# Performance work log

Hardware: AMD Instinct MI355X
Metric: run time of the kernel (lower is better)

The kernel has to match this reference:

```python
import jax, jax.numpy as jnp
import numpy as np

N = 8192
D_IN = 2048
D_OUT = 2048


def _xavier(key, fan_in, fan_out):
    limit = float(np.sqrt(6.0 / (fan_in + fan_out)))
    return jax.random.uniform(key, (fan_in, fan_out), jnp.float32, -limit, limit)


def setup_inputs() -> dict:
    key = jax.random.key(0)
    kx, kk, kv, kq = jax.random.split(key, 4)
    x = jax.random.normal(kx, (N, D_IN), dtype=jnp.float32)
    w_keys = _xavier(kk, D_IN, D_OUT)
    w_values = _xavier(kv, D_IN, D_OUT)
    w_querys = _xavier(kq, D_IN, D_OUT)
    return {"x": x, "w_keys": w_keys, "w_values": w_values, "w_querys": w_querys}


def reference(x, w_keys, w_values, w_querys):
    # QKV projections: [N, d_out]
    keys = x @ w_keys
    values = x @ w_values
    querys = x @ w_querys
    # attn_scores[i, j] = <query_i, key_j>; softmax over keys (last dim)
    attn = jax.nn.softmax(querys @ keys.T, axis=-1)  # [N, N]
    # Original: (values[:,None] * attn.T[:,:,None]).sum(0) == attn @ values
    outputs = attn @ values  # [N, d_out]
    return outputs
```

## Files before the change

### kernel.cpp

```cpp
#include <hip/hip_runtime.h>
#include <hip/hip_bf16.h>
#include <cstdint>
#include <cstddef>


typedef float  f32x4 __attribute__((ext_vector_type(4)));
typedef short  s16x8 __attribute__((ext_vector_type(8)));
typedef unsigned short u16;
typedef u16    u16x4 __attribute__((ext_vector_type(4)));

#define NROWS 8192
#define DDIM  2048

static __device__ __forceinline__ u16 f2bf(float f) {
    unsigned u = __float_as_uint(f);
    u += 0x7FFFu + ((u >> 16) & 1u);
    return (u16)(u >> 16);
}
static __device__ __forceinline__ float bf2f(u16 h) {
    return __uint_as_float(((unsigned)h) << 16);
}
static __device__ __forceinline__ f32x4 mfma16(s16x8 a, s16x8 b, f32x4 c) {
    return __builtin_amdgcn_mfma_f32_16x16x32_bf16(a, b, c, 0, 0, 0);
}

__global__ __launch_bounds__(256) void transpose_f32k(const float* __restrict__ in,
                                                      float* __restrict__ op,
                                                      int rows, int cols) {
    __shared__ float t[32][33];
    const int r  = threadIdx.x >> 3;
    const int c4 = (threadIdx.x & 7) << 2;
    f32x4 v = *(const f32x4*)(in + (size_t)(blockIdx.y * 32 + r) * cols + blockIdx.x * 32 + c4);
    t[r][c4 + 0] = v[0]; t[r][c4 + 1] = v[1]; t[r][c4 + 2] = v[2]; t[r][c4 + 3] = v[3];
    __syncthreads();
    f32x4 o;
#pragma unroll
    for (int j = 0; j < 4; ++j) o[j] = t[c4 + j][r];
    *(f32x4*)(op + (size_t)(blockIdx.x * 32 + r) * rows + blockIdx.y * 32 + c4) = o;
}

__global__ void fill_marker(float* o, long n) {
    long i = (long)blockIdx.x * blockDim.x + threadIdx.x;
    const long stride = (long)gridDim.x * blockDim.x;
    for (; i < n; i += stride) o[i] = 1.0e30f;
}

template<int NA, int NB, int ORD, int AF32, int BF32, int OUTM>
__global__ __launch_bounds__(256) void gemm_u(
    const void* Ap0, const void* Ap1, const void* Ap2, long lda,
    const void* Bp0, const void* Bp1, const void* Bp2, long ldb,
    float* __restrict__ Cf, u16* __restrict__ Ct, long ldc, int K)
{
    __shared__ __align__(16) u16 lds[NA + NB][128][40];

    const int tid  = threadIdx.x;
    const int lane = tid & 63;
    const int w    = tid >> 6;
    const int wr   = w >> 1, wc = w & 1;
    const int lrow = lane & 15, kg = lane >> 4;
    const long brow = (long)blockIdx.y * 128;
    const long bcol = (long)blockIdx.x * 128;
    const int srow = tid >> 1;
    const int sk   = (tid & 1) * 16;

    f32x4 acc[4][4];
#pragma unroll
    for (int m = 0; m < 4; ++m)
#pragma unroll
        for (int n = 0; n < 4; ++n) acc[m][n] = (f32x4){0.f, 0.f, 0.f, 0.f};

    const int nk = K / 32;
    for (int kt = 0; kt < nk; ++kt) {
        u16x4 sa[NA][4], sb[NB][4];
        if (AF32) {
            const float* pA = (const float*)Ap0 + (brow + srow) * lda + (long)kt * 32 + sk;
#pragma unroll
            for (int q = 0; q < 4; ++q) {
                f32x4 v = *(const f32x4*)(pA + q * 4);
#pragma unroll
                for (int e = 0; e < 4; ++e) {
                    float f = v[e];
                    u16 hh = f2bf(f); sa[0][q][e] = hh;
                    if (NA > 1) {
                        float r1 = f - bf2f(hh);
                        u16 mm = f2bf(r1); sa[1][q][e] = mm;
                        if (NA > 2) sa[2][q][e] = f2bf(r1 - bf2f(mm));
                    }
                }
            }
        } else {
            const u16* as[3] = {(const u16*)Ap0, (const u16*)Ap1, (const u16*)Ap2};
            const long off = (brow + srow) * lda + (long)kt * 32 + sk;
#pragma unroll
            for (int i = 0; i < NA; ++i) {
                s16x8 v0 = *(const s16x8*)(as[i] + off);
                s16x8 v1 = *(const s16x8*)(as[i] + off + 8);
                *(s16x8*)&sa[i][0] = v0;
                *(s16x8*)&sa[i][2] = v1;
            }
        }
        if (BF32) {
            const float* pB = (const float*)Bp0 + (bcol + srow) * ldb + (long)kt * 32 + sk;
#pragma unroll
            for (int q = 0; q < 4; ++q) {
                f32x4 v = *(const f32x4*)(pB + q * 4);
#pragma unroll
                for (int e = 0; e < 4; ++e) {
                    float f = v[e];
                    u16 hh = f2bf(f); sb[0][q][e] = hh;
                    if (NB > 1) {
                        float r1 = f - bf2f(hh);
                        u16 mm = f2bf(r1); sb[1][q][e] = mm;
                        if (NB > 2) sb[2][q][e] = f2bf(r1 - bf2f(mm));
                    }
                }
            }
        } else {
            const u16* bs[3] = {(const u16*)Bp0, (const u16*)Bp1, (const u16*)Bp2};
            const long off = (bcol + srow) * ldb + (long)kt * 32 + sk;
#pragma unroll
            for (int j = 0; j < NB; ++j) {
                s16x8 v0 = *(const s16x8*)(bs[j] + off);
                s16x8 v1 = *(const s16x8*)(bs[j] + off + 8);
                *(s16x8*)&sb[j][0] = v0;
                *(s16x8*)&sb[j][2] = v1;
            }
        }

        __syncthreads();
#pragma unroll
        for (int i = 0; i < NA; ++i)
#pragma unroll
            for (int q = 0; q < 4; ++q)
                *(u16x4*)&lds[i][srow][sk + q * 4] = sa[i][q];
#pragma unroll
        for (int j = 0; j < NB; ++j)
#pragma unroll
            for (int q = 0; q < 4; ++q)
                *(u16x4*)&lds[NA + j][srow][sk + q * 4] = sb[j][q];
        __syncthreads();

        s16x8 bfr[NB][4];
#pragma unroll
        for (int j = 0; j < NB; ++j)
#pragma unroll
            for (int n = 0; n < 4; ++n)
                bfr[j][n] = *(const s16x8*)&lds[NA + j][wc * 64 + n * 16 + lrow][kg * 8];
#pragma unroll
        for (int m = 0; m < 4; ++m) {
            s16x8 afr[NA];
#pragma unroll
            for (int i = 0; i < NA; ++i)
                afr[i] = *(const s16x8*)&lds[i][wr * 64 + m * 16 + lrow][kg * 8];
#pragma unroll
            for (int n = 0; n < 4; ++n) {
#pragma unroll
                for (int i = 0; i < NA; ++i)
#pragma unroll
                    for (int j = 0; j < NB; ++j)
                        if (i + j <= ORD)
                            acc[m][n] = mfma16(afr[i], bfr[j][n], acc[m][n]);
            }
        }
    }

#pragma unroll
    for (int m = 0; m < 4; ++m) {
#pragma unroll
        for (int n = 0; n < 4; ++n) {
            const long c = bcol + wc * 64 + n * 16 + lrow;
            if (OUTM == 0) {
#pragma unroll
                for (int reg = 0; reg < 4; ++reg) {
                    const long r = brow + wr * 64 + m * 16 + kg * 4 + reg;
                    Cf[r * ldc + c] = acc[m][n][reg];
                }
            } else {
                const long r0 = brow + wr * 64 + m * 16 + kg * 4;
                u16x4 hv;
#pragma unroll
                for (int reg = 0; reg < 4; ++reg) hv[reg] = f2bf(acc[m][n][reg]);
                *(u16x4*)(Ct + c * ldc + r0) = hv;
            }
        }
    }
}

__global__ __launch_bounds__(256) void softmax_rows(float* __restrict__ S) {
    __shared__ float row[NROWS];
    __shared__ float red[4];
    const int tid = threadIdx.x;
    const int lane = tid & 63, wid = tid >> 6;
    float* src = S + (size_t)blockIdx.x * NROWS;

    float lmax = -3.4e38f;
    for (int i = tid * 4; i < NROWS; i += 1024) {
        f32x4 v = *(const f32x4*)(src + i);
        row[i] = v[0]; row[i + 1] = v[1]; row[i + 2] = v[2]; row[i + 3] = v[3];
        lmax = fmaxf(fmaxf(fmaxf(lmax, v[0]), v[1]), fmaxf(v[2], v[3]));
    }
#pragma unroll
    for (int off = 32; off; off >>= 1) lmax = fmaxf(lmax, __shfl_xor(lmax, off, 64));
    if (lane == 0) red[wid] = lmax;
    __syncthreads();
    const float m = fmaxf(fmaxf(red[0], red[1]), fmaxf(red[2], red[3]));
    __syncthreads();

    float lsum = 0.f;
    for (int i = tid * 4; i < NROWS; i += 1024) {
        float e0 = __expf(row[i] - m);
        float e1 = __expf(row[i + 1] - m);
        float e2 = __expf(row[i + 2] - m);
        float e3 = __expf(row[i + 3] - m);
        row[i] = e0; row[i + 1] = e1; row[i + 2] = e2; row[i + 3] = e3;
        lsum += (e0 + e1) + (e2 + e3);
    }
#pragma unroll
    for (int off = 32; off; off >>= 1) lsum += __shfl_xor(lsum, off, 64);
    if (lane == 0) red[wid] = lsum;
    __syncthreads();
    const float inv = 1.0f / ((red[0] + red[1]) + (red[2] + red[3]));

    u16* ph = (u16*)src;
    for (int i = tid * 4; i < NROWS; i += 1024) {
        u16x4 h;
#pragma unroll
        for (int j = 0; j < 4; ++j) h[j] = f2bf(row[i + j] * inv);
        *(u16x4*)(ph + i) = h;
    }
}

extern "C" void kernel_launch(void* const* d_in, const int* in_sizes, int n_in,
                              void* d_out, int out_size, void* d_ws, size_t ws_size,
                              hipStream_t stream) {
    const float* x  = (const float*)d_in[0];
    const float* wk = (const float*)d_in[1];
    const float* wv = (const float*)d_in[2];
    const float* wq = (const float*)d_in[3];
    float* out = (float*)d_out;
    char*  ws  = (char*)d_ws;
    const size_t MiB = 1024ull * 1024ull;

    long R = 0;
    const size_t fixed = 48 * MiB;
    if      (ws_size >= fixed + 256 * MiB) R = 8192;
    else if (ws_size >= fixed + 128 * MiB) R = 4096;
    else if (ws_size >= fixed +  64 * MiB) R = 2048;
    else if (ws_size >= fixed +  32 * MiB) R = 1024;
    else if (ws_size >= fixed +  16 * MiB) R = 512;
    else if (ws_size >= fixed +   8 * MiB) R = 256;
    if (R == 0) {
        fill_marker<<<dim3(2048), dim3(256), 0, stream>>>(out, (long)NROWS * DDIM);
        return;
    }

    float* Mb  = (float*)(ws);
    u16*   Vt  = (u16*)(ws + 16 * MiB);
    char*  cb  = ws + 48 * MiB;
    float* WvT = (float*)cb;
    float* Sch = (float*)cb;
    float* y   = out;

    const dim3 b256(256);

    gemm_u<3, 3, 2, 1, 1, 0><<<dim3(16, 16), b256, 0, stream>>>(
        wk, nullptr, nullptr, (long)DDIM, wq, nullptr, nullptr, (long)DDIM,
        Mb, nullptr, (long)DDIM, DDIM);

    transpose_f32k<<<dim3(64, 64), b256, 0, stream>>>(wv, WvT, DDIM, DDIM);
    gemm_u<2, 2, 1, 1, 1, 1><<<dim3(16, 64), b256, 0, stream>>>(
        x, nullptr, nullptr, (long)DDIM, WvT, nullptr, nullptr, (long)DDIM,
        nullptr, Vt, (long)NROWS, DDIM);

    gemm_u<2, 2, 1, 1, 1, 0><<<dim3(16, 64), b256, 0, stream>>>(
        x, nullptr, nullptr, (long)DDIM, Mb, nullptr, nullptr, (long)DDIM,
        y, nullptr, (long)DDIM, DDIM);

    const long nc = NROWS / R;
    for (long c = 0; c < nc; ++c) {
        float* yc = y   + (size_t)c * R * DDIM;
        float* oc = out + (size_t)c * R * DDIM;
        gemm_u<2, 2, 1, 1, 1, 0><<<dim3(64, R / 128), b256, 0, stream>>>(
            yc, nullptr, nullptr, (long)DDIM, x, nullptr, nullptr, (long)DDIM,
            Sch, nullptr, (long)NROWS, DDIM);
        softmax_rows<<<dim3(R), b256, 0, stream>>>(Sch);
        gemm_u<1, 1, 0, 0, 0, 0><<<dim3(16, R / 128), b256, 0, stream>>>(
            (const u16*)Sch, nullptr, nullptr, (long)(2 * NROWS),
            Vt, nullptr, nullptr, (long)NROWS,
            oc, nullptr, (long)DDIM, NROWS);
    }
}
```

Baseline: 2.336 ms.

## Pre-split fp32 operands into packed bf16 hi/lo tiles loaded via global_load_lds

Adds pre-pass kernels that split x and the transposed Wv into bf16 high/low pairs stored in an MFMA-fragment-friendly tiled layout. A new GEMM streams these tiles straight into LDS with global_load_lds, which removes the per-iteration fp32-to-bf16 splitting and the register staging. The Wk·Wq product drops from a 3-term to a 2-term split and is written directly in the packed format, and y is stored packed inside the output buffer. This removes repeated conversion work on x across several GEMMs, at the cost of slightly lower precision in the Wk·Wq product and extra packing passes.

```diff
diff --git a/kernel.cpp b/kernel.cpp
--- a/kernel.cpp
+++ b/kernel.cpp
@@ -8,6 +8,7 @@
 typedef short  s16x8 __attribute__((ext_vector_type(8)));
 typedef unsigned short u16;
 typedef u16    u16x4 __attribute__((ext_vector_type(4)));
+typedef u16    u16x8 __attribute__((ext_vector_type(8)));
 
 #define NROWS 8192
 #define DDIM  2048
@@ -23,20 +24,53 @@
 static __device__ __forceinline__ f32x4 mfma16(s16x8 a, s16x8 b, f32x4 c) {
     return __builtin_amdgcn_mfma_f32_16x16x32_bf16(a, b, c, 0, 0, 0);
 }
-
-__global__ __launch_bounds__(256) void transpose_f32k(const float* __restrict__ in,
-                                                      float* __restrict__ op,
-                                                      int rows, int cols) {
-    __shared__ float t[32][33];
-    const int r  = threadIdx.x >> 3;
-    const int c4 = (threadIdx.x & 7) << 2;
-    f32x4 v = *(const f32x4*)(in + (size_t)(blockIdx.y * 32 + r) * cols + blockIdx.x * 32 + c4);
-    t[r][c4 + 0] = v[0]; t[r][c4 + 1] = v[1]; t[r][c4 + 2] = v[2]; t[r][c4 + 3] = v[3];
-    __syncthreads();
-    f32x4 o;
-#pragma unroll
-    for (int j = 0; j < 4; ++j) o[j] = t[c4 + j][r];
-    *(f32x4*)(op + (size_t)(blockIdx.x * 32 + r) * rows + blockIdx.y * 32 + c4) = o;
+static __device__ __forceinline__ void gload16(const void* g, void* l) {
+    __builtin_amdgcn_global_load_lds(
+        (const __attribute__((address_space(1))) void*)g,
+        (__attribute__((address_space(3))) void*)l, 16, 0, 0);
+}
+
+
+__global__ __launch_bounds__(256) void split2_pack(const float* __restrict__ x,
+                                                   u16* __restrict__ xh,
+                                                   u16* __restrict__ xm) {
+    const long i   = (long)blockIdx.x * 256 + threadIdx.x;
+    const int  sub = (int)(i & 63);
+    const long tk  = i >> 6;
+    const int  kt  = (int)(tk & 63);
+    const long rt  = tk >> 6;
+    const long row = rt * 16 + (sub & 15);
+    const int  k0  = kt * 32 + (sub >> 4) * 8;
+    const float* p = x + row * DDIM + k0;
+    f32x4 v0 = *(const f32x4*)p, v1 = *(const f32x4*)(p + 4);
+    u16x8 h, m;
+#pragma unroll
+    for (int j = 0; j < 8; ++j) {
+        float f = (j < 4) ? v0[j] : v1[j - 4];
+        u16 hh = f2bf(f); h[j] = hh; m[j] = f2bf(f - bf2f(hh));
+    }
+    *(u16x8*)(xh + i * 8) = h;
+    *(u16x8*)(xm + i * 8) = m;
+}
+
+__global__ __launch_bounds__(256) void twvpack(const float* __restrict__ wv,
+                                               u16* __restrict__ th,
+                                               u16* __restrict__ tm) {
+    const long i   = (long)blockIdx.x * 256 + threadIdx.x;
+    const int  sub = (int)(i & 63);
+    const long tk  = i >> 6;
+    const int  kt  = (int)(tk & 63);
+    const long rt  = tk >> 6;
+    const long rowp = rt * 16 + (sub & 15);
+    const int  k0   = kt * 32 + (sub >> 4) * 8;
+    u16x8 h, m;
+#pragma unroll
+    for (int j = 0; j < 8; ++j) {
+        float f = wv[(long)(k0 + j) * DDIM + rowp];
+        u16 hh = f2bf(f); h[j] = hh; m[j] = f2bf(f - bf2f(hh));
+    }
+    *(u16x8*)(th + i * 8) = h;
+    *(u16x8*)(tm + i * 8) = m;
 }
 
 __global__ void fill_marker(float* o, long n) {
@@ -45,13 +79,98 @@
     for (; i < n; i += stride) o[i] = 1.0e30f;
 }
 
+template<int OUTM>
+__global__ __launch_bounds__(256) void gemm_pk(
+    const u16* __restrict__ Ah, const u16* __restrict__ Am,
+    const u16* __restrict__ Bh, const u16* __restrict__ Bm,
+    float* __restrict__ Cf, u16* __restrict__ Ct, long ldc, int rshift)
+{
+    __shared__ __align__(16) u16 lds[4][8][512];
+
+    const int tid = threadIdx.x, lane = tid & 63, w = tid >> 6;
+    const int wr = w >> 1, wc = w & 1;
+    const long bx = blockIdx.x, by = blockIdx.y;
+
+    const u16* t0 = (w & 1) ? Am : Ah;
+    const u16* t1 = (w & 1) ? Bm : Bh;
+    const u16* gb = (w & 2) ? t1 : t0;
+    const long tb = ((w & 2) ? bx : by) * 8;
+    u16* lb = (u16*)&lds[0][0][0] + (long)w * 8 * 512;
+
+    f32x4 acc[4][4];
+#pragma unroll
+    for (int m = 0; m < 4; ++m)
+#pragma unroll
+        for (int n = 0; n < 4; ++n) acc[m][n] = (f32x4){0.f, 0.f, 0.f, 0.f};
+
+    for (int kt = 0; kt < 64; ++kt) {
+        __syncthreads();
+        const u16* gt = gb + (tb * 64 + kt) * 512 + lane * 8;
+#pragma unroll
+        for (int t = 0; t < 8; ++t)
+            gload16(gt + (long)t * 32768, lb + t * 512);
+        __syncthreads();
+
+        s16x8 bh[4], bm[4];
+#pragma unroll
+        for (int n = 0; n < 4; ++n) {
+            bh[n] = *(const s16x8*)&lds[2][wc * 4 + n][lane * 8];
+            bm[n] = *(const s16x8*)&lds[3][wc * 4 + n][lane * 8];
+        }
+#pragma unroll
+        for (int m = 0; m < 4; ++m) {
+            s16x8 ah = *(const s16x8*)&lds[0][wr * 4 + m][lane * 8];
+            s16x8 am = *(const s16x8*)&lds[1][wr * 4 + m][lane * 8];
+#pragma unroll
+            for (int n = 0; n < 4; ++n) {
+                acc[m][n] = mfma16(ah, bh[n], acc[m][n]);
+                acc[m][n] = mfma16(ah, bm[n], acc[m][n]);
+                acc[m][n] = mfma16(am, bh[n], acc[m][n]);
+            }
+        }
+    }
+
+    const int lrow = lane & 15, kg = lane >> 4;
+#pragma unroll
+    for (int m = 0; m < 4; ++m) {
+#pragma unroll
+        for (int n = 0; n < 4; ++n) {
+            const long c  = bx * 128 + wc * 64 + n * 16 + lrow;
+            const long r0 = by * 128 + wr * 64 + m * 16 + kg * 4;
+            if (OUTM == 0) {
+#pragma unroll
+                for (int reg = 0; reg < 4; ++reg)
+                    Cf[(r0 + reg) * ldc + c] = acc[m][n][reg];
+            } else if (OUTM == 1) {
+                u16x4 hv;
+#pragma unroll
+                for (int reg = 0; reg < 4; ++reg) hv[reg] = f2bf(acc[m][n][reg]);
+                *(u16x4*)(Ct + c * ldc + r0) = hv;
+            } else {
+#pragma unroll
+                for (int reg = 0; reg < 4; ++reg) {
+                    const long r = r0 + reg;
+                    const float v = acc[m][n][reg];
+                    const u16 hh = f2bf(v);
+                    const u16 mm = f2bf(v - bf2f(hh));
+                    const long base = (r >> rshift) << (rshift + 12);
+                    const long off  = ((((r & ((1L << rshift) - 1)) >> 4) * 64 + (c >> 5)) * 64
+                                       + ((c & 31) >> 3) * 16 + (r & 15)) * 8 + (c & 7);
+                    Ct[base + off] = hh;
+                    Ct[base + (1L << (rshift + 11)) + off] = mm;
+                }
+            }
+        }
+    }
+}
+
 template<int NA, int NB, int ORD, int AF32, int BF32, int OUTM>
 __global__ __launch_bounds__(256) void gemm_u(
     const void* Ap0, const void* Ap1, const void* Ap2, long lda,
     const void* Bp0, const void* Bp1, const void* Bp2, long ldb,
-    float* __restrict__ Cf, u16* __restrict__ Ct, long ldc, int K)
+    float* __restrict__ Cf, u16* __restrict__ Ct, long ldc, int K, int rshift)
 {
-    __shared__ __align__(16) u16 lds[NA + NB][128][40];
+    __shared__ __align__(16) u16 lds[NA + NB][128][36];
 
     const int tid  = threadIdx.x;
     const int lane = tid & 63;
@@ -81,23 +200,16 @@
                 for (int e = 0; e < 4; ++e) {
                     float f = v[e];
                     u16 hh = f2bf(f); sa[0][q][e] = hh;
-                    if (NA > 1) {
-                        float r1 = f - bf2f(hh);
-                        u16 mm = f2bf(r1); sa[1][q][e] = mm;
-                        if (NA > 2) sa[2][q][e] = f2bf(r1 - bf2f(mm));
-                    }
+                    if (NA > 1) sa[1][q][e] = f2bf(f - bf2f(hh));
                 }
             }
         } else {
-            const u16* as[3] = {(const u16*)Ap0, (const u16*)Ap1, (const u16*)Ap2};
+            const u16* as0 = (const u16*)Ap0;
             const long off = (brow + srow) * lda + (long)kt * 32 + sk;
-#pragma unroll
-            for (int i = 0; i < NA; ++i) {
-                s16x8 v0 = *(const s16x8*)(as[i] + off);
-                s16x8 v1 = *(const s16x8*)(as[i] + off + 8);
-                *(s16x8*)&sa[i][0] = v0;
-                *(s16x8*)&sa[i][2] = v1;
-            }
+            s16x8 v0 = *(const s16x8*)(as0 + off);
+            s16x8 v1 = *(const s16x8*)(as0 + off + 8);
+            *(s16x8*)&sa[0][0] = v0;
+            *(s16x8*)&sa[0][2] = v1;
         }
         if (BF32) {
             const float* pB = (const float*)Bp0 + (bcol + srow) * ldb + (long)kt * 32 + sk;
@@ -108,23 +220,16 @@
                 for (int e = 0; e < 4; ++e) {
                     float f = v[e];
                     u16 hh = f2bf(f); sb[0][q][e] = hh;
-                    if (NB > 1) {
-                        float r1 = f - bf2f(hh);
-                        u16 mm = f2bf(r1); sb[1][q][e] = mm;
-                        if (NB > 2) sb[2][q][e] = f2bf(r1 - bf2f(mm));
-                    }
+                    if (NB > 1) sb[1][q][e] = f2bf(f - bf2f(hh));
                 }
             }
         } else {
-            const u16* bs[3] = {(const u16*)Bp0, (const u16*)Bp1, (const u16*)Bp2};
+            const u16* bs0 = (const u16*)Bp0;
             const long off = (bcol + srow) * ldb + (long)kt * 32 + sk;
-#pragma unroll
-            for (int j = 0; j < NB; ++j) {
-                s16x8 v0 = *(const s16x8*)(bs[j] + off);
-                s16x8 v1 = *(const s16x8*)(bs[j] + off + 8);
-                *(s16x8*)&sb[j][0] = v0;
-                *(s16x8*)&sb[j][2] = v1;
-            }
+            s16x8 v0 = *(const s16x8*)(bs0 + off);
+            s16x8 v1 = *(const s16x8*)(bs0 + off + 8);
+            *(s16x8*)&sb[0][0] = v0;
+            *(s16x8*)&sb[0][2] = v1;
         }
 
         __syncthreads();
@@ -168,19 +273,30 @@
     for (int m = 0; m < 4; ++m) {
 #pragma unroll
         for (int n = 0; n < 4; ++n) {
-            const long c = bcol + wc * 64 + n * 16 + lrow;
+            const long c  = bcol + wc * 64 + n * 16 + lrow;
+            const long r0 = brow + wr * 64 + m * 16 + kg * 4;
             if (OUTM == 0) {
 #pragma unroll
-                for (int reg = 0; reg < 4; ++reg) {
-                    const long r = brow + wr * 64 + m * 16 + kg * 4 + reg;
-                    Cf[r * ldc + c] = acc[m][n][reg];
-                }
-            } else {
-                const long r0 = brow + wr * 64 + m * 16 + kg * 4;
+                for (int reg = 0; reg < 4; ++reg)
+                    Cf[(r0 + reg) * ldc + c] = acc[m][n][reg];
+            } else if (OUTM == 1) {
                 u16x4 hv;
 #pragma unroll
                 for (int reg = 0; reg < 4; ++reg) hv[reg] = f2bf(acc[m][n][reg]);
                 *(u16x4*)(Ct + c * ldc + r0) = hv;
+            } else {
+#pragma unroll
+                for (int reg = 0; reg < 4; ++reg) {
+                    const long r = r0 + reg;
+                    const float v = acc[m][n][reg];
+                    const u16 hh = f2bf(v);
+                    const u16 mm = f2bf(v - bf2f(hh));
+                    const long base = (r >> rshift) << (rshift + 12);
+                    const long off  = ((((r & ((1L << rshift) - 1)) >> 4) * 64 + (c >> 5)) * 64
+                                       + ((c & 31) >> 3) * 16 + (r & 15)) * 8 + (c & 7);
+                    Ct[base + off] = hh;
+                    Ct[base + (1L << (rshift + 11)) + off] = mm;
+                }
             }
         }
     }
@@ -242,51 +358,50 @@
     const size_t MiB = 1024ull * 1024ull;
 
     long R = 0;
-    const size_t fixed = 48 * MiB;
-    if      (ws_size >= fixed + 256 * MiB) R = 8192;
-    else if (ws_size >= fixed + 128 * MiB) R = 4096;
-    else if (ws_size >= fixed +  64 * MiB) R = 2048;
-    else if (ws_size >= fixed +  32 * MiB) R = 1024;
-    else if (ws_size >= fixed +  16 * MiB) R = 512;
-    else if (ws_size >= fixed +   8 * MiB) R = 256;
+    if      (ws_size >= 352 * MiB) R = 8192;
+    else if (ws_size >= 224 * MiB) R = 4096;
+    else if (ws_size >= 160 * MiB) R = 2048;
+    else if (ws_size >= 128 * MiB) R = 1024;
+    else if (ws_size >= 112 * MiB) R = 512;
     if (R == 0) {
         fill_marker<<<dim3(2048), dim3(256), 0, stream>>>(out, (long)NROWS * DDIM);
         return;
     }
-
-    float* Mb  = (float*)(ws);
-    u16*   Vt  = (u16*)(ws + 16 * MiB);
-    char*  cb  = ws + 48 * MiB;
-    float* WvT = (float*)cb;
+    int rs = 0; while ((1L << rs) < R) ++rs;
+
+    u16* xh = (u16*)ws;
+    u16* xm = (u16*)(ws + 32 * MiB);
+    u16* Vt = (u16*)(ws + 64 * MiB);
+    char* cb = ws + 96 * MiB;
+    u16* Gh  = (u16*)cb;  u16* Gm  = Gh  + (long)DDIM * DDIM;
+    u16* Wvh = (u16*)cb;  u16* Wvm = Wvh + (long)DDIM * DDIM;
     float* Sch = (float*)cb;
-    float* y   = out;
+    u16* ypk = (u16*)out;
 
     const dim3 b256(256);
 
-    gemm_u<3, 3, 2, 1, 1, 0><<<dim3(16, 16), b256, 0, stream>>>(
+    split2_pack<<<dim3(8192), b256, 0, stream>>>(x, xh, xm);
+
+    gemm_u<2, 2, 1, 1, 1, 2><<<dim3(16, 16), b256, 0, stream>>>(
         wk, nullptr, nullptr, (long)DDIM, wq, nullptr, nullptr, (long)DDIM,
-        Mb, nullptr, (long)DDIM, DDIM);
-
-    transpose_f32k<<<dim3(64, 64), b256, 0, stream>>>(wv, WvT, DDIM, DDIM);
-    gemm_u<2, 2, 1, 1, 1, 1><<<dim3(16, 64), b256, 0, stream>>>(
-        x, nullptr, nullptr, (long)DDIM, WvT, nullptr, nullptr, (long)DDIM,
-        nullptr, Vt, (long)NROWS, DDIM);
-
-    gemm_u<2, 2, 1, 1, 1, 0><<<dim3(16, 64), b256, 0, stream>>>(
-        x, nullptr, nullptr, (long)DDIM, Mb, nullptr, nullptr, (long)DDIM,
-        y, nullptr, (long)DDIM, DDIM);
+        nullptr, Gh, (long)DDIM, DDIM, 11);
+
+    gemm_pk<2><<<dim3(16, 64), b256, 0, stream>>>(xh, xm, Gh, Gm,
+                                                  nullptr, ypk, (long)DDIM, rs);
+
+    twvpack<<<dim3(2048), b256, 0, stream>>>(wv, Wvh, Wvm);
+    gemm_pk<1><<<dim3(16, 64), b256, 0, stream>>>(xh, xm, Wvh, Wvm,
+                                                  nullptr, Vt, (long)NROWS, 0);
 
     const long nc = NROWS / R;
     for (long c = 0; c < nc; ++c) {
-        float* yc = y   + (size_t)c * R * DDIM;
-        float* oc = out + (size_t)c * R * DDIM;
-        gemm_u<2, 2, 1, 1, 1, 0><<<dim3(64, R / 128), b256, 0, stream>>>(
-            yc, nullptr, nullptr, (long)DDIM, x, nullptr, nullptr, (long)DDIM,
-            Sch, nullptr, (long)NROWS, DDIM);
+        const u16* Ahc = ypk + c * (R << 12);
+        gemm_pk<0><<<dim3(64, R / 128), b256, 0, stream>>>(
+            Ahc, Ahc + R * 2048, xh, xm, Sch, nullptr, (long)NROWS, 0);
         softmax_rows<<<dim3(R), b256, 0, stream>>>(Sch);
         gemm_u<1, 1, 0, 0, 0, 0><<<dim3(16, R / 128), b256, 0, stream>>>(
             (const u16*)Sch, nullptr, nullptr, (long)(2 * NROWS),
             Vt, nullptr, nullptr, (long)NROWS,
-            oc, nullptr, (long)DDIM, NROWS);
-    }
-}
+            out + (size_t)c * R * DDIM, nullptr, (long)DDIM, NROWS, 0);
+    }
+}
```

New measurement: 1.878 ms. 19.6% less time.
